# Optimization experiments

Hardware: AMD Instinct MI355X
Metric: run time of the kernel (lower is better)

## Reference

```python
import jax, jax.numpy as jnp
import numpy as np

N_NODES = 50000


def gcn_conv(h, W, b, src, dst, n_nodes):
    # PyG GCNConv: h' = D^{-1/2} (A + I) D^{-1/2} (h @ W) + b
    h = h @ W  # [N, out]
    deg = jax.ops.segment_sum(jnp.ones_like(dst, dtype=h.dtype), dst, num_segments=n_nodes)
    dinv = jnp.where(deg > 0, jax.lax.rsqrt(deg), 0.0)  # [N]
    norm = dinv[src] * dinv[dst]  # [E]
    msg = h[src] * norm[:, None]  # [E, out]
    out = jax.ops.segment_sum(msg, dst, num_segments=n_nodes)
    return out + b


def setup_inputs() -> dict:
    key = jax.random.key(0)
    ks = jax.random.split(key, 12)
    N, E, P, D, H = N_NODES, 1600000, 200000, 128, 128
    s = lambda fan_in: 1.0 / np.sqrt(fan_in)
    return {
        "x": jax.random.normal(ks[0], (N, D), dtype=jnp.float32),
        "edge_index": jax.random.randint(ks[1], (2, E), 0, N, dtype=jnp.int32),
        "drug_pairs": jax.random.randint(ks[2], (P, 2), 0, N, dtype=jnp.int32),
        "W1": jax.random.normal(ks[3], (D, H), dtype=jnp.float32) * s(D),
        "b1": jnp.zeros((H,), dtype=jnp.float32),
        "W2": jax.random.normal(ks[4], (H, H), dtype=jnp.float32) * s(H),
        "b2": jnp.zeros((H,), dtype=jnp.float32),
        "Wh1": jax.random.normal(ks[5], (2 * H, H), dtype=jnp.float32) * s(2 * H),
        "bh1": jnp.zeros((H,), dtype=jnp.float32),
        "Wh2": jax.random.normal(ks[6], (H, 1), dtype=jnp.float32) * s(H),
        "bh2": jnp.zeros((1,), dtype=jnp.float32),
    }


def reference(x, edge_index, drug_pairs, W1, b1, W2, b2, Wh1, bh1, Wh2, bh2):
    n = x.shape[0]
    # add self-loops once (GCNConv default add_self_loops=True)
    loop = jnp.arange(n, dtype=edge_index.dtype)
    src = jnp.concatenate([edge_index[0], loop])
    dst = jnp.concatenate([edge_index[1], loop])

    h = jax.nn.relu(gcn_conv(x, W1, b1, src, dst, n))  # dropout = identity (eval)
    h = jax.nn.relu(gcn_conv(h, W2, b2, src, dst, n))

    combined = jnp.concatenate([h[drug_pairs[:, 0]], h[drug_pairs[:, 1]]], axis=1)  # [P, 2H]
    out = jax.nn.relu(combined @ Wh1 + bh1) @ Wh2 + bh2  # [P, 1]
    return out
```

## Files before the change

kernel.cpp:

```cpp
#include <hip/hip_runtime.h>
#include <hip/hip_fp16.h>


#define BSH 9
#define BSZ (1 << BSH)
#define MSB 4096
#define XPAD 132

typedef __attribute__((ext_vector_type(8))) short bf16x8;
typedef __attribute__((ext_vector_type(4))) float f32x4;

__global__ __launch_bounds__(256) void k_zero_i32(int* __restrict__ p, int n) {
  int i = blockIdx.x * 256 + threadIdx.x;
  if (i < n) p[i] = 0;
}

__global__ __launch_bounds__(256) void k_bucket_hist(const int* __restrict__ dst,
                                                     int* __restrict__ gcnt,
                                                     int e, int kb) {
  __shared__ int h[128];
  int tid = threadIdx.x;
  if (tid < kb) h[tid] = 0;
  __syncthreads();
  int stride = gridDim.x * 256;
  for (int i = blockIdx.x * 256 + tid; i < e; i += stride) {
    int d = __builtin_nontemporal_load(&dst[i]);
    atomicAdd(&h[d >> BSH], 1);
  }
  __syncthreads();
  if (tid < kb) atomicAdd(&gcnt[tid], h[tid]);
}

__global__ __launch_bounds__(128) void k_bucket_scan(const int* __restrict__ gcnt,
                                                     int* __restrict__ gbase,
                                                     int* __restrict__ gcur,
                                                     int kb) {
  __shared__ int ws[2];
  int t = threadIdx.x;
  int lane = t & 63, w = t >> 6;
  int v = (t < kb) ? gcnt[t] : 0;
  int orig = v;
#pragma unroll
  for (int o = 1; o < 64; o <<= 1) {
    int u = __shfl_up(v, o, 64);
    if (lane >= o) v += u;
  }
  if (lane == 63) ws[w] = v;
  __syncthreads();
  int ex = ((w == 1) ? ws[0] : 0) + v - orig;
  if (t < kb) { gbase[t] = ex; gcur[t] = ex; }
  if (t == kb - 1) gbase[kb] = ex + orig;
}

__global__ __launch_bounds__(256) void k_multisplit(const int* __restrict__ src,
                                                    const int* __restrict__ dst,
                                                    int* __restrict__ gcur,
                                                    int* __restrict__ tmp,
                                                    int e, int kb) {
  __shared__ int h[128], base[128];
  int tid = threadIdx.x;
  if (tid < kb) h[tid] = 0;
  __syncthreads();
  int i0 = blockIdx.x * MSB + tid;
  int d[16], rk[16];
#pragma unroll
  for (int u = 0; u < 16; ++u) {
    int i = i0 + u * 256;
    if (i < e) {
      d[u] = __builtin_nontemporal_load(&dst[i]);
      rk[u] = atomicAdd(&h[d[u] >> BSH], 1);
    }
  }
  __syncthreads();
  if (tid < kb && h[tid] > 0) base[tid] = atomicAdd(&gcur[tid], h[tid]);
  __syncthreads();
#pragma unroll
  for (int u = 0; u < 16; ++u) {
    int i = i0 + u * 256;
    if (i < e) {
      int s = __builtin_nontemporal_load(&src[i]);
      tmp[base[d[u] >> BSH] + rk[u]] = ((d[u] & (BSZ - 1)) << 16) | s;
    }
  }
}

__global__ __launch_bounds__(512) void k_bucket_build(
    const int* __restrict__ tmp, const int* __restrict__ gbase,
    int* __restrict__ rowptr, float* __restrict__ dinv,
    unsigned short* __restrict__ colarr, int n, int kb, int e) {
  __shared__ int dl[BSZ], cl[BSZ], ws[8];
  int t = threadIdx.x, b = blockIdx.x;
  int s0 = gbase[b], s1 = gbase[b + 1];
  dl[t] = 0;
  __syncthreads();
  for (int j = s0 + t; j < s1; j += 512)
    atomicAdd(&dl[((unsigned)tmp[j]) >> 16], 1);
  __syncthreads();
  int lane = t & 63, w = t >> 6;
  int v = dl[t], orig = v;
#pragma unroll
  for (int o = 1; o < 64; o <<= 1) {
    int u = __shfl_up(v, o, 64);
    if (lane >= o) v += u;
  }
  if (lane == 63) ws[w] = v;
  __syncthreads();
  if (t == 0) {
    int a = 0;
#pragma unroll
    for (int k = 0; k < 8; ++k) { int x = ws[k]; ws[k] = a; a += x; }
  }
  __syncthreads();
  int ex = ws[w] + v - orig;
  cl[t] = ex;
  int node = (b << BSH) + t;
  if (node < n) {
    rowptr[node] = s0 + ex;
    dinv[node] = rsqrtf((float)(orig + 1));
  }
  if (b == kb - 1 && t == 0) rowptr[n] = e;
  __syncthreads();
  for (int j = s0 + t; j < s1; j += 512) {
    int p = tmp[j];
    int r = atomicAdd(&cl[((unsigned)p) >> 16], 1);
    colarr[s0 + r] = (unsigned short)(p & 0xFFFF);
  }
}

__device__ __forceinline__ void split8(const float* v, bf16x8& hi, bf16x8& lo) {
#pragma unroll
  for (int j = 0; j < 8; ++j) {
    unsigned u = __float_as_uint(v[j]);
    hi[j] = (short)(u >> 16);
    float lf = v[j] - __uint_as_float(u & 0xffff0000u);
    lo[j] = (short)(__float_as_uint(lf) >> 16);
  }
}

__global__ __launch_bounds__(256) void k_prep_w(
    const float* __restrict__ W1, const float* __restrict__ W2,
    const float* __restrict__ Wh1, short* __restrict__ fragH,
    short* __restrict__ fragL) {
  int g = blockIdx.x * 256 + threadIdx.x;
  if (g >= 4 * 2048) return;
  int w = g >> 11;
  int rem = g & 2047;
  int lane = rem & 63;
  int ts = rem >> 6;
  int t = ts >> 2, s = ts & 3;
  int n = (t << 4) + (lane & 15);
  int k0 = s * 32 + (lane >> 4) * 8;
  const float* W = (w == 0) ? W1 : (w == 1) ? W2 : (w == 2) ? Wh1 : (Wh1 + 128 * 128);
  short h[8], l[8];
#pragma unroll
  for (int j = 0; j < 8; ++j) {
    float x = W[(k0 + j) * 128 + n];
    unsigned u = __float_as_uint(x);
    h[j] = (short)(u >> 16);
    float lf = x - __uint_as_float(u & 0xffff0000u);
    l[j] = (short)(__float_as_uint(lf) >> 16);
  }
  ((int4*)fragH)[g] = *(int4*)h;
  ((int4*)fragL)[g] = *(int4*)l;
}

__global__ __launch_bounds__(256) void k_gemm_mfma(
    const float* __restrict__ X, const short* __restrict__ fragH,
    const short* __restrict__ fragL, const float* __restrict__ rowscale,
    __half* __restrict__ C16, int n) {
  __shared__ float sX[64 * XPAD];
  int tid = threadIdx.x;
  int row0 = blockIdx.x * 64;
  const float2* X2 = (const float2*)(X + (size_t)row0 * 128);
#pragma unroll
  for (int it = 0; it < 16; ++it) {
    int t = it * 256 + tid;
    int r = t >> 6, c2 = t & 63;
    int gr = row0 + r;
    float2 v = (gr < n) ? X2[t] : make_float2(0.f, 0.f);
    *(float2*)&sX[r * XPAD + c2 * 2] = v;
  }
  __syncthreads();
  int wid = tid >> 6, lane = tid & 63;
  int r0 = row0 + wid * 16;
  if (r0 >= n) return;
  int m = lane & 15, quad = lane >> 4;
  const float* xrow = sX + (wid * 16 + m) * XPAD;
  f32x4 acc[8];
#pragma unroll
  for (int t = 0; t < 8; ++t) acc[t] = (f32x4)(0.f);
  const int4* FH = (const int4*)fragH;
  const int4* FL = (const int4*)fragL;
#pragma unroll
  for (int s = 0; s < 4; ++s) {
    int k0 = s * 32 + quad * 8;
    float xv[8];
    *(float2*)&xv[0] = *(const float2*)(xrow + k0);
    *(float2*)&xv[2] = *(const float2*)(xrow + k0 + 2);
    *(float2*)&xv[4] = *(const float2*)(xrow + k0 + 4);
    *(float2*)&xv[6] = *(const float2*)(xrow + k0 + 6);
    bf16x8 ah, al;
    split8(xv, ah, al);
#pragma unroll
    for (int t = 0; t < 8; ++t) {
      int idx = (t * 4 + s) * 64 + lane;
      bf16x8 bh = *(const bf16x8*)&FH[idx];
      bf16x8 bl = *(const bf16x8*)&FL[idx];
      acc[t] = __builtin_amdgcn_mfma_f32_16x16x32_bf16(ah, bh, acc[t], 0, 0, 0);
      acc[t] = __builtin_amdgcn_mfma_f32_16x16x32_bf16(al, bh, acc[t], 0, 0, 0);
      acc[t] = __builtin_amdgcn_mfma_f32_16x16x32_bf16(ah, bl, acc[t], 0, 0, 0);
    }
  }
  float sc[4];
#pragma unroll
  for (int r = 0; r < 4; ++r)
    sc[r] = rowscale ? rowscale[r0 + quad * 4 + r] : 1.f;
#pragma unroll
  for (int t = 0; t < 8; ++t) {
#pragma unroll
    for (int r = 0; r < 4; ++r) {
      int row = r0 + quad * 4 + r;
      C16[(size_t)row * 128 + t * 16 + m] = __float2half(acc[t][r] * sc[r]);
    }
  }
}

__global__ __launch_bounds__(256) void k_agg_h(
    const __half2* __restrict__ g2, const float* __restrict__ dinv,
    const int* __restrict__ rowptr, const unsigned short* __restrict__ col,
    const float* __restrict__ bias, float* __restrict__ out, int n) {
  int i = blockIdx.x * 4 + (threadIdx.x >> 6);
  int c = threadIdx.x & 63;
  if (i >= n) return;
  float2 a0 = __half22float2(g2[(size_t)i * 64 + c]);
  float2 a1 = make_float2(0.f, 0.f);
  float2 a2 = make_float2(0.f, 0.f);
  float2 a3 = make_float2(0.f, 0.f);
  int beg = rowptr[i], end = rowptr[i + 1];
  int j = beg;
  for (; j + 4 <= end; j += 4) {
    int s0 = __builtin_nontemporal_load(&col[j]);
    int s1 = __builtin_nontemporal_load(&col[j + 1]);
    int s2 = __builtin_nontemporal_load(&col[j + 2]);
    int s3 = __builtin_nontemporal_load(&col[j + 3]);
    float2 v0 = __half22float2(g2[(size_t)s0 * 64 + c]);
    float2 v1 = __half22float2(g2[(size_t)s1 * 64 + c]);
    float2 v2 = __half22float2(g2[(size_t)s2 * 64 + c]);
    float2 v3 = __half22float2(g2[(size_t)s3 * 64 + c]);
    a0.x += v0.x; a0.y += v0.y;
    a1.x += v1.x; a1.y += v1.y;
    a2.x += v2.x; a2.y += v2.y;
    a3.x += v3.x; a3.y += v3.y;
  }
  for (; j < end; ++j) {
    int s0 = __builtin_nontemporal_load(&col[j]);
    float2 v = __half22float2(g2[(size_t)s0 * 64 + c]);
    a0.x += v.x; a0.y += v.y;
  }
  float di = dinv[i];
  float2 bi = ((const float2*)bias)[c];
  float2 o;
  o.x = fmaxf(fmaf(di, (a0.x + a1.x) + (a2.x + a3.x), bi.x), 0.f);
  o.y = fmaxf(fmaf(di, (a0.y + a1.y) + (a2.y + a3.y), bi.y), 0.f);
  ((float2*)out)[(size_t)i * 64 + c] = o;
}

__global__ __launch_bounds__(256) void k_pairs_h(
    const __half2* __restrict__ A, const __half2* __restrict__ B,
    const int* __restrict__ pairs, const float* __restrict__ bh1,
    const float* __restrict__ wh2, const float* __restrict__ bh2,
    float* __restrict__ out, int P) {
  int p = blockIdx.x * 4 + (threadIdx.x >> 6);
  int c = threadIdx.x & 63;
  if (p >= P) return;
  int p0 = pairs[2 * p], p1 = pairs[2 * p + 1];
  float2 av = __half22float2(A[(size_t)p0 * 64 + c]);
  float2 bv = __half22float2(B[(size_t)p1 * 64 + c]);
  float2 bi = ((const float2*)bh1)[c];
  float2 wv = ((const float2*)wh2)[c];
  float v0 = fmaxf(av.x + bv.x + bi.x, 0.f) * wv.x;
  float v1 = fmaxf(av.y + bv.y + bi.y, 0.f) * wv.y;
  float s = v0 + v1;
#pragma unroll
  for (int o = 32; o > 0; o >>= 1) s += __shfl_down(s, o, 64);
  if (c == 0) out[p] = s + bh2[0];
}

extern "C" void kernel_launch(void* const* d_in, const int* in_sizes, int n_in,
                              void* d_out, int out_size, void* d_ws, size_t ws_size,
                              hipStream_t stream) {
  const float* x   = (const float*)d_in[0];
  const int* ei    = (const int*)d_in[1];
  const int* pairs = (const int*)d_in[2];
  const float* W1  = (const float*)d_in[3];
  const float* b1  = (const float*)d_in[4];
  const float* W2  = (const float*)d_in[5];
  const float* b2  = (const float*)d_in[6];
  const float* Wh1 = (const float*)d_in[7];
  const float* bh1 = (const float*)d_in[8];
  const float* Wh2 = (const float*)d_in[9];
  const float* bh2 = (const float*)d_in[10];
  (void)n_in; (void)out_size; (void)ws_size;

  int N = in_sizes[0] / 128;
  int E = in_sizes[1] / 2;
  int P = in_sizes[2] / 2;
  const int* src = ei;
  const int* dst = ei + E;
  int KB = (N + BSZ - 1) >> BSH;

  char* wsp = (char*)d_ws;
  size_t off = 0;
  auto alloc = [&](size_t bytes) -> void* {
    void* p = wsp + off;
    off += (bytes + 255) & ~(size_t)255;
    return p;
  };
  __half* g16 = (__half*)alloc((size_t)N * 128 * 2);
  float* h1   = (float*)alloc((size_t)N * 128 * 4);
  float* h2   = (float*)alloc((size_t)N * 128 * 4);
  float* dinv = (float*)alloc((size_t)N * 4);
  int* rowptr = (int*)alloc((size_t)(N + 1) * 4);
  unsigned short* colarr = (unsigned short*)alloc((size_t)E * 2);
  int* tmp    = (int*)alloc((size_t)E * 4);
  short* fragH = (short*)alloc(4 * 2048 * 8 * 2);
  short* fragL = (short*)alloc(4 * 2048 * 8 * 2);
  int* gcnt  = (int*)alloc((size_t)(KB + 1) * 4);
  int* gbase = (int*)alloc((size_t)(KB + 1) * 4);
  int* gcur  = (int*)alloc((size_t)(KB + 1) * 4);
  __half* A16 = g16;
  __half* B16 = (__half*)h1;
  short* fH_W1 = fragH + 0 * 16384;  short* fL_W1 = fragL + 0 * 16384;
  short* fH_W2 = fragH + 1 * 16384;  short* fL_W2 = fragL + 1 * 16384;
  short* fH_Wa = fragH + 2 * 16384;  short* fL_Wa = fragL + 2 * 16384;
  short* fH_Wb = fragH + 3 * 16384;  short* fL_Wb = fragL + 3 * 16384;

  k_prep_w<<<32, 256, 0, stream>>>(W1, W2, Wh1, fragH, fragL);

  k_zero_i32<<<1, 256, 0, stream>>>(gcnt, KB + 1);
  k_bucket_hist<<<256, 256, 0, stream>>>(dst, gcnt, E, KB);
  k_bucket_scan<<<1, 128, 0, stream>>>(gcnt, gbase, gcur, KB);
  k_multisplit<<<(E + MSB - 1) / MSB, 256, 0, stream>>>(src, dst, gcur, tmp, E, KB);
  k_bucket_build<<<KB, 512, 0, stream>>>(tmp, gbase, rowptr, dinv, colarr, N, KB, E);

  int GB = (N + 63) / 64;
  int AB = (N + 3) / 4;
  k_gemm_mfma<<<GB, 256, 0, stream>>>(x, fH_W1, fL_W1, dinv, g16, N);
  k_agg_h<<<AB, 256, 0, stream>>>((const __half2*)g16, dinv, rowptr, colarr, b1, h1, N);
  k_gemm_mfma<<<GB, 256, 0, stream>>>(h1, fH_W2, fL_W2, dinv, g16, N);
  k_agg_h<<<AB, 256, 0, stream>>>((const __half2*)g16, dinv, rowptr, colarr, b2, h2, N);
  k_gemm_mfma<<<GB, 256, 0, stream>>>(h2, fH_Wa, fL_Wa, nullptr, A16, N);
  k_gemm_mfma<<<GB, 256, 0, stream>>>(h2, fH_Wb, fL_Wb, nullptr, B16, N);
  k_pairs_h<<<(P + 3) / 4, 256, 0, stream>>>((const __half2*)A16, (const __half2*)B16,
                                             pairs, bh1, Wh2, bh2, (float*)d_out, P);
}
```

Measured before the change: 404.5 us.

## Fuse dual head GEMMs and widen gather loads to 8-byte half4

Replaces the two head-projection GEMM launches with one kernel that loads h2 into shared memory once and computes both A and B outputs. The aggregation kernel now has each half-wave read 8-byte half4 chunks and process alternating neighbours, combining the halves with a cross-half shuffle. The pair kernel loads A and B rows in the two half-waves and combines them with an xor shuffle. This aims to cut launches, redundant reads of h2 and per-lane load instruction count, at the cost of extra shuffles and higher register use in the fused GEMM.

```diff
diff --git a/kernel.cpp b/kernel.cpp
--- a/kernel.cpp
+++ b/kernel.cpp
@@ -9,6 +9,12 @@
 
 typedef __attribute__((ext_vector_type(8))) short bf16x8;
 typedef __attribute__((ext_vector_type(4))) float f32x4;
+
+__device__ __forceinline__ float4 h4_to_f4(uint2 u) {
+  float2 fa = __half22float2(*(__half2*)&u.x);
+  float2 fb = __half22float2(*(__half2*)&u.y);
+  return make_float4(fa.x, fa.y, fb.x, fb.y);
+}
 
 __global__ __launch_bounds__(256) void k_zero_i32(int* __restrict__ p, int n) {
   int i = blockIdx.x * 256 + threadIdx.x;
@@ -225,44 +231,127 @@
   }
 }
 
+__global__ __launch_bounds__(256) void k_gemm_dual(
+    const float* __restrict__ X,
+    const short* __restrict__ fHa, const short* __restrict__ fLa,
+    const short* __restrict__ fHb, const short* __restrict__ fLb,
+    __half* __restrict__ A16, __half* __restrict__ B16, int n) {
+  __shared__ float sX[64 * XPAD];
+  int tid = threadIdx.x;
+  int row0 = blockIdx.x * 64;
+  const float2* X2 = (const float2*)(X + (size_t)row0 * 128);
+#pragma unroll
+  for (int it = 0; it < 16; ++it) {
+    int t = it * 256 + tid;
+    int r = t >> 6, c2 = t & 63;
+    int gr = row0 + r;
+    float2 v = (gr < n) ? X2[t] : make_float2(0.f, 0.f);
+    *(float2*)&sX[r * XPAD + c2 * 2] = v;
+  }
+  __syncthreads();
+  int wid = tid >> 6, lane = tid & 63;
+  int r0 = row0 + wid * 16;
+  if (r0 >= n) return;
+  int m = lane & 15, quad = lane >> 4;
+  const float* xrow = sX + (wid * 16 + m) * XPAD;
+  f32x4 accA[8], accB[8];
+#pragma unroll
+  for (int t = 0; t < 8; ++t) { accA[t] = (f32x4)(0.f); accB[t] = (f32x4)(0.f); }
+  const int4* FHa = (const int4*)fHa; const int4* FLa = (const int4*)fLa;
+  const int4* FHb = (const int4*)fHb; const int4* FLb = (const int4*)fLb;
+#pragma unroll
+  for (int s = 0; s < 4; ++s) {
+    int k0 = s * 32 + quad * 8;
+    float xv[8];
+    *(float2*)&xv[0] = *(const float2*)(xrow + k0);
+    *(float2*)&xv[2] = *(const float2*)(xrow + k0 + 2);
+    *(float2*)&xv[4] = *(const float2*)(xrow + k0 + 4);
+    *(float2*)&xv[6] = *(const float2*)(xrow + k0 + 6);
+    bf16x8 ah, al;
+    split8(xv, ah, al);
+#pragma unroll
+    for (int t = 0; t < 8; ++t) {
+      int idx = (t * 4 + s) * 64 + lane;
+      bf16x8 bha = *(const bf16x8*)&FHa[idx];
+      bf16x8 bla = *(const bf16x8*)&FLa[idx];
+      accA[t] = __builtin_amdgcn_mfma_f32_16x16x32_bf16(ah, bha, accA[t], 0, 0, 0);
+      accA[t] = __builtin_amdgcn_mfma_f32_16x16x32_bf16(al, bha, accA[t], 0, 0, 0);
+      accA[t] = __builtin_amdgcn_mfma_f32_16x16x32_bf16(ah, bla, accA[t], 0, 0, 0);
+      bf16x8 bhb = *(const bf16x8*)&FHb[idx];
+      bf16x8 blb = *(const bf16x8*)&FLb[idx];
+      accB[t] = __builtin_amdgcn_mfma_f32_16x16x32_bf16(ah, bhb, accB[t], 0, 0, 0);
+      accB[t] = __builtin_amdgcn_mfma_f32_16x16x32_bf16(al, bhb, accB[t], 0, 0, 0);
+      accB[t] = __builtin_amdgcn_mfma_f32_16x16x32_bf16(ah, blb, accB[t], 0, 0, 0);
+    }
+  }
+#pragma unroll
+  for (int t = 0; t < 8; ++t) {
+#pragma unroll
+    for (int r = 0; r < 4; ++r) {
+      int row = r0 + quad * 4 + r;
+      A16[(size_t)row * 128 + t * 16 + m] = __float2half(accA[t][r]);
+      B16[(size_t)row * 128 + t * 16 + m] = __float2half(accB[t][r]);
+    }
+  }
+}
+
 __global__ __launch_bounds__(256) void k_agg_h(
     const __half2* __restrict__ g2, const float* __restrict__ dinv,
     const int* __restrict__ rowptr, const unsigned short* __restrict__ col,
     const float* __restrict__ bias, float* __restrict__ out, int n) {
   int i = blockIdx.x * 4 + (threadIdx.x >> 6);
-  int c = threadIdx.x & 63;
   if (i >= n) return;
-  float2 a0 = __half22float2(g2[(size_t)i * 64 + c]);
-  float2 a1 = make_float2(0.f, 0.f);
-  float2 a2 = make_float2(0.f, 0.f);
-  float2 a3 = make_float2(0.f, 0.f);
+  int lane = threadIdx.x & 63;
+  int sub = lane >> 5;
+  int c4 = lane & 31;
+  const uint2* G4 = (const uint2*)g2;
+  float4 a0 = make_float4(0.f, 0.f, 0.f, 0.f), a1 = a0, a2 = a0, a3 = a0;
+  if (sub == 0) a0 = h4_to_f4(G4[(size_t)i * 32 + c4]);
   int beg = rowptr[i], end = rowptr[i + 1];
   int j = beg;
-  for (; j + 4 <= end; j += 4) {
+  for (; j + 8 <= end; j += 8) {
+    int s0 = __builtin_nontemporal_load(&col[j + 0 + sub]);
+    int s1 = __builtin_nontemporal_load(&col[j + 2 + sub]);
+    int s2 = __builtin_nontemporal_load(&col[j + 4 + sub]);
+    int s3 = __builtin_nontemporal_load(&col[j + 6 + sub]);
+    float4 v0 = h4_to_f4(G4[(size_t)s0 * 32 + c4]);
+    float4 v1 = h4_to_f4(G4[(size_t)s1 * 32 + c4]);
+    float4 v2 = h4_to_f4(G4[(size_t)s2 * 32 + c4]);
+    float4 v3 = h4_to_f4(G4[(size_t)s3 * 32 + c4]);
+    a0.x += v0.x; a0.y += v0.y; a0.z += v0.z; a0.w += v0.w;
+    a1.x += v1.x; a1.y += v1.y; a1.z += v1.z; a1.w += v1.w;
+    a2.x += v2.x; a2.y += v2.y; a2.z += v2.z; a2.w += v2.w;
+    a3.x += v3.x; a3.y += v3.y; a3.z += v3.z; a3.w += v3.w;
+  }
+  for (; j + 2 <= end; j += 2) {
+    int s0 = __builtin_nontemporal_load(&col[j + sub]);
+    float4 v = h4_to_f4(G4[(size_t)s0 * 32 + c4]);
+    a0.x += v.x; a0.y += v.y; a0.z += v.z; a0.w += v.w;
+  }
+  if (j < end && sub == 0) {
     int s0 = __builtin_nontemporal_load(&col[j]);
-    int s1 = __builtin_nontemporal_load(&col[j + 1]);
-    int s2 = __builtin_nontemporal_load(&col[j + 2]);
-    int s3 = __builtin_nontemporal_load(&col[j + 3]);
-    float2 v0 = __half22float2(g2[(size_t)s0 * 64 + c]);
-    float2 v1 = __half22float2(g2[(size_t)s1 * 64 + c]);
-    float2 v2 = __half22float2(g2[(size_t)s2 * 64 + c]);
-    float2 v3 = __half22float2(g2[(size_t)s3 * 64 + c]);
-    a0.x += v0.x; a0.y += v0.y;
-    a1.x += v1.x; a1.y += v1.y;
-    a2.x += v2.x; a2.y += v2.y;
-    a3.x += v3.x; a3.y += v3.y;
-  }
-  for (; j < end; ++j) {
-    int s0 = __builtin_nontemporal_load(&col[j]);
-    float2 v = __half22float2(g2[(size_t)s0 * 64 + c]);
-    a0.x += v.x; a0.y += v.y;
-  }
-  float di = dinv[i];
-  float2 bi = ((const float2*)bias)[c];
-  float2 o;
-  o.x = fmaxf(fmaf(di, (a0.x + a1.x) + (a2.x + a3.x), bi.x), 0.f);
-  o.y = fmaxf(fmaf(di, (a0.y + a1.y) + (a2.y + a3.y), bi.y), 0.f);
-  ((float2*)out)[(size_t)i * 64 + c] = o;
+    float4 v = h4_to_f4(G4[(size_t)s0 * 32 + c4]);
+    a0.x += v.x; a0.y += v.y; a0.z += v.z; a0.w += v.w;
+  }
+  float4 s;
+  s.x = (a0.x + a1.x) + (a2.x + a3.x);
+  s.y = (a0.y + a1.y) + (a2.y + a3.y);
+  s.z = (a0.z + a1.z) + (a2.z + a3.z);
+  s.w = (a0.w + a1.w) + (a2.w + a3.w);
+  s.x += __shfl_down(s.x, 32, 64);
+  s.y += __shfl_down(s.y, 32, 64);
+  s.z += __shfl_down(s.z, 32, 64);
+  s.w += __shfl_down(s.w, 32, 64);
+  if (sub == 0) {
+    float di = dinv[i];
+    float4 bi = ((const float4*)bias)[c4];
+    float4 o;
+    o.x = fmaxf(fmaf(di, s.x, bi.x), 0.f);
+    o.y = fmaxf(fmaf(di, s.y, bi.y), 0.f);
+    o.z = fmaxf(fmaf(di, s.z, bi.z), 0.f);
+    o.w = fmaxf(fmaf(di, s.w, bi.w), 0.f);
+    ((float4*)out)[(size_t)i * 32 + c4] = o;
+  }
 }
 
 __global__ __launch_bounds__(256) void k_pairs_h(
@@ -271,19 +360,24 @@
     const float* __restrict__ wh2, const float* __restrict__ bh2,
     float* __restrict__ out, int P) {
   int p = blockIdx.x * 4 + (threadIdx.x >> 6);
-  int c = threadIdx.x & 63;
+  int lane = threadIdx.x & 63;
   if (p >= P) return;
+  int sub = lane >> 5, c4 = lane & 31;
   int p0 = pairs[2 * p], p1 = pairs[2 * p + 1];
-  float2 av = __half22float2(A[(size_t)p0 * 64 + c]);
-  float2 bv = __half22float2(B[(size_t)p1 * 64 + c]);
-  float2 bi = ((const float2*)bh1)[c];
-  float2 wv = ((const float2*)wh2)[c];
-  float v0 = fmaxf(av.x + bv.x + bi.x, 0.f) * wv.x;
-  float v1 = fmaxf(av.y + bv.y + bi.y, 0.f) * wv.y;
-  float s = v0 + v1;
-#pragma unroll
-  for (int o = 32; o > 0; o >>= 1) s += __shfl_down(s, o, 64);
-  if (c == 0) out[p] = s + bh2[0];
+  const uint2* T4 = sub ? (const uint2*)B : (const uint2*)A;
+  int row = sub ? p1 : p0;
+  float4 v = h4_to_f4(T4[(size_t)row * 32 + c4]);
+  v.x += __shfl_xor(v.x, 32, 64);
+  v.y += __shfl_xor(v.y, 32, 64);
+  v.z += __shfl_xor(v.z, 32, 64);
+  v.w += __shfl_xor(v.w, 32, 64);
+  float4 bi = ((const float4*)bh1)[c4];
+  float4 wv = ((const float4*)wh2)[c4];
+  float s = fmaxf(v.x + bi.x, 0.f) * wv.x + fmaxf(v.y + bi.y, 0.f) * wv.y +
+            fmaxf(v.z + bi.z, 0.f) * wv.z + fmaxf(v.w + bi.w, 0.f) * wv.w;
+#pragma unroll
+  for (int o = 16; o > 0; o >>= 1) s += __shfl_down(s, o, 64);
+  if (lane == 0) out[p] = s + bh2[0];
 }
 
 extern "C" void kernel_launch(void* const* d_in, const int* in_sizes, int n_in,
@@ -349,8 +443,7 @@
   k_agg_h<<<AB, 256, 0, stream>>>((const __half2*)g16, dinv, rowptr, colarr, b1, h1, N);
   k_gemm_mfma<<<GB, 256, 0, stream>>>(h1, fH_W2, fL_W2, dinv, g16, N);
   k_agg_h<<<AB, 256, 0, stream>>>((const __half2*)g16, dinv, rowptr, colarr, b2, h2, N);
-  k_gemm_mfma<<<GB, 256, 0, stream>>>(h2, fH_Wa, fL_Wa, nullptr, A16, N);
-  k_gemm_mfma<<<GB, 256, 0, stream>>>(h2, fH_Wb, fL_Wb, nullptr, B16, N);
+  k_gemm_dual<<<GB, 256, 0, stream>>>(h2, fH_Wa, fL_Wa, fH_Wb, fL_Wb, A16, B16, N);
   k_pairs_h<<<(P + 3) / 4, 256, 0, stream>>>((const __half2*)A16, (const __half2*)B16,
                                              pairs, bh1, Wh2, bh2, (float*)d_out, P);
 }
```

After: 385.5 us. 4.7% less time.
